# Performance work log

Hardware: AMD Instinct MI355X
Metric: run time of the kernel (lower is better)

Reference implementation:

```python
import jax, jax.numpy as jnp
import numpy as np

B, N, DIM, H, DH = 2, 2048, 1024, 16, 64
SCALE = 8.0
LN_EPS = 1e-5
L2_EPS = 1e-12


def setup_inputs() -> dict:
    key = jax.random.key(0)
    ks = jax.random.split(key, 6)
    s = 0.02  # keep projections at sane magnitude
    return {
        "x": jax.random.normal(ks[0], (B, N, DIM), dtype=jnp.float32),
        "g": jnp.ones((DIM,), dtype=jnp.float32),
        "b": jnp.zeros((DIM,), dtype=jnp.float32),
        "c_attn_w": jax.random.normal(ks[1], (DIM, 3 * DIM), dtype=jnp.float32) * s,
        "c_attn_b": jax.random.normal(ks[2], (3 * DIM,), dtype=jnp.float32) * s,
        "c_proj_w": jax.random.normal(ks[3], (DIM, DIM), dtype=jnp.float32) * s,
        "c_proj_b": jax.random.normal(ks[4], (DIM,), dtype=jnp.float32) * s,
        "to_out_w": jax.random.normal(ks[5], (DIM, DIM), dtype=jnp.float32) * s,
    }


def _l2norm(t):
    # F.normalize(t, dim=-1): t / max(||t||, eps)
    n = jnp.sqrt(jnp.sum(t * t, axis=-1, keepdims=True))
    return t / jnp.maximum(n, L2_EPS)


def reference(x, g, b, c_attn_w, c_attn_b, c_proj_w, c_proj_b, to_out_w):
    # LayerNorm
    mu = jnp.mean(x, axis=-1, keepdims=True)
    var = jnp.mean(jnp.square(x - mu), axis=-1, keepdims=True)
    y = (x - mu) * jax.lax.rsqrt(var + LN_EPS) * g + b  # [B,N,DIM]

    # GPT2 Conv1D c_attn: y @ W + b, split into q/k/v
    qkv = y @ c_attn_w + c_attn_b  # [B,N,3*DIM]
    q, k, v = jnp.split(qkv, 3, axis=-1)

    def split_heads(t):
        return t.reshape(B, N, H, DH).transpose(0, 2, 1, 3)  # [B,H,N,DH]

    q, k, v = split_heads(q), split_heads(k), split_heads(v)

    # cosine-sim attention: L2-normalize q,k, scaled dot product, causal softmax
    qn, kn = _l2norm(q), _l2norm(k)
    sim = jnp.einsum("bhid,bhjd->bhij", qn, kn) * SCALE  # [B,H,N,N]
    mask_value = -jnp.finfo(sim.dtype).max
    causal = jnp.triu(jnp.ones((N, N), dtype=bool), k=1)
    sim = jnp.where(causal, mask_value, sim)
    attn = jax.nn.softmax(sim, axis=-1)
    o = jnp.einsum("bhij,bhjd->bhid", attn, v)  # [B,H,N,DH]

    o = o.transpose(0, 2, 1, 3).reshape(B, N, DIM)
    o = o @ c_proj_w + c_proj_b          # Conv1D c_proj
    out = o @ to_out_w.T                  # Linear to_out (no bias)
    return out
```

## Files before the change

### kernel.cpp

```cpp
#include <hip/hip_runtime.h>
#include <cstdint>
#include <cstddef>

#define Bb 2
#define Nn 2048
#define DIMM 1024
#define Hh 16
#define DHh 64
#define BH (Bb*Hh)
#define MROWS (Bb*Nn)

typedef __bf16 bf16x8 __attribute__((ext_vector_type(8)));
typedef float f32x4 __attribute__((ext_vector_type(4)));
typedef short s16x4 __attribute__((ext_vector_type(4)));

__device__ __forceinline__ unsigned short f2bf(float f) {
  unsigned u = __float_as_uint(f);
  u += 0x7FFFu + ((u >> 16) & 1u);
  return (unsigned short)(u >> 16);
}
__device__ __forceinline__ unsigned short f2bf_fast(float f) {
  return (unsigned short)((__float_as_uint(f) + 0x8000u) >> 16);
}
__device__ __forceinline__ float bf2f(unsigned short s) {
  return __uint_as_float(((unsigned)s) << 16);
}

#define GLDS16(g, l) __builtin_amdgcn_global_load_lds( \
    (const __attribute__((address_space(1))) void*)(g), \
    (__attribute__((address_space(3))) void*)(l), 16, 0, 0)

__global__ __launch_bounds__(256) void prep_kernel(
    const float* __restrict__ x, const float* __restrict__ g,
    const float* __restrict__ b,
    const float* __restrict__ c_attn_w, const float* __restrict__ c_proj_w,
    const float* __restrict__ to_out_w, const float* __restrict__ c_proj_b,
    unsigned short* __restrict__ y,
    unsigned short* __restrict__ wqkv, unsigned short* __restrict__ wpbf,
    unsigned short* __restrict__ wout, float* __restrict__ bc) {
  int bid = blockIdx.x;
  int t = threadIdx.x;
  if (bid < 4096) {
    int row = bid;
    const float4* xr = (const float4*)(x + (size_t)row * DIMM);
    float4 v = xr[t];
    float s  = v.x + v.y + v.z + v.w;
    float ss = v.x*v.x + v.y*v.y + v.z*v.z + v.w*v.w;
    #pragma unroll
    for (int o = 1; o < 64; o <<= 1) { s += __shfl_xor(s, o); ss += __shfl_xor(ss, o); }
    __shared__ float red[8];
    int wv = t >> 6;
    if ((t & 63) == 0) { red[wv] = s; red[wv + 4] = ss; }
    __syncthreads();
    s  = red[0] + red[1] + red[2] + red[3];
    ss = red[4] + red[5] + red[6] + red[7];
    float mu  = s * (1.0f / DIMM);
    float var = ss * (1.0f / DIMM) - mu * mu;
    float rs  = rsqrtf(var + 1e-5f);
    float4 gv = ((const float4*)g)[t];
    float4 bv = ((const float4*)b)[t];
    ushort4 o4;
    o4.x = f2bf((v.x - mu) * rs * gv.x + bv.x);
    o4.y = f2bf((v.y - mu) * rs * gv.y + bv.y);
    o4.z = f2bf((v.z - mu) * rs * gv.z + bv.z);
    o4.w = f2bf((v.w - mu) * rs * gv.w + bv.w);
    ((ushort4*)y)[(size_t)row * 256 + t] = o4;
  } else if (bid < 7168) {
    __shared__ float tile[32][33];
    int bb = bid - 4096;
    int bx = bb % 96, by = bb / 96;
    int tx = t & 31, ty = t >> 5;
    int x2 = bx * 32 + tx;
    int y0 = by * 32;
    #pragma unroll
    for (int j = 0; j < 32; j += 8)
      tile[ty + j][tx] = c_attn_w[(size_t)(y0 + ty + j) * 3072 + x2];
    __syncthreads();
    int ox  = by * 32 + tx;
    int oy0 = bx * 32;
    #pragma unroll
    for (int j = 0; j < 32; j += 8)
      wqkv[(size_t)(oy0 + ty + j) * 1024 + ox] = f2bf(tile[tx][ty + j]);
  } else if (bid < 9216) {
    bool iswp = bid < 8192;
    int bb = bid - (iswp ? 7168 : 8192);
    const float* in = iswp ? c_proj_w : to_out_w;
    unsigned short* out = iswp ? wpbf : wout;
    int i = (bb * 256 + t) * 4;
    float4 v = *(const float4*)(in + i);
    ushort4 o;
    o.x = f2bf(v.x); o.y = f2bf(v.y); o.z = f2bf(v.z); o.w = f2bf(v.w);
    *(ushort4*)(out + i) = o;
  } else {
    int n = (bid - 9216) * 4 + (t >> 6);
    int lane = t & 63;
    const float4* w = (const float4*)(to_out_w + (size_t)n * DIMM);
    const float4* b4 = (const float4*)c_proj_b;
    float s = 0.0f;
    #pragma unroll
    for (int k = 0; k < 4; k++) {
      float4 wv = w[lane + k * 64], bv = b4[lane + k * 64];
      s += wv.x * bv.x + wv.y * bv.y + wv.z * bv.z + wv.w * bv.w;
    }
    #pragma unroll
    for (int o = 1; o < 64; o <<= 1) s += __shfl_xor(s, o);
    if (lane == 0) bc[n] = s;
  }
}

template <int EPI>
__device__ __forceinline__ void gemm_body(
    const unsigned short* __restrict__ A, const unsigned short* __restrict__ Bt,
    const float* __restrict__ bias,
    unsigned short* __restrict__ obf, float* __restrict__ of32,
    unsigned short* __restrict__ q_std, unsigned short* __restrict__ k_std,
    unsigned short* __restrict__ vt_out,
    int M, int N, int K, int bn, int bm,
    unsigned short* smem) {
  unsigned short* sA = smem;
  unsigned short* sB = smem + 128 * 64;
  int t = threadIdx.x;
  int lane = t & 63, wv = t >> 6;
  int wm = (wv >> 1) * 64, wn = (wv & 1) * 64;
  int l16 = lane & 15, quad = lane >> 4;

  const unsigned short* Ab = A + (size_t)(bm * 128) * K;
  const unsigned short* Bb2 = Bt + (size_t)(bn * 128) * K;
  int srow = t >> 3;
  int gch = (t & 7) ^ (srow & 7);

  f32x4 acc[4][4] = {};

  for (int kt = 0; kt < K; kt += 64) {
    __syncthreads();
    #pragma unroll
    for (int i = 0; i < 4; i++) {
      GLDS16(Ab  + (size_t)(srow + 32 * i) * K + kt + gch * 8, sA + (size_t)(t + 256 * i) * 8);
      GLDS16(Bb2 + (size_t)(srow + 32 * i) * K + kt + gch * 8, sB + (size_t)(t + 256 * i) * 8);
    }
    __syncthreads();
    #pragma unroll
    for (int kk = 0; kk < 2; kk++) {
      int slot = (kk * 4 + quad) ^ (l16 & 7);
      bf16x8 af[4], bfr[4];
      #pragma unroll
      for (int i = 0; i < 4; i++)
        af[i] = *(const bf16x8*)(sA + (size_t)(wm + i * 16 + l16) * 64 + slot * 8);
      #pragma unroll
      for (int j = 0; j < 4; j++)
        bfr[j] = *(const bf16x8*)(sB + (size_t)(wn + j * 16 + l16) * 64 + slot * 8);
      #pragma unroll
      for (int i = 0; i < 4; i++)
        #pragma unroll
        for (int j = 0; j < 4; j++)
          acc[i][j] = __builtin_amdgcn_mfma_f32_16x16x32_bf16(af[i], bfr[j], acc[i][j], 0, 0, 0);
    }
  }

  float bvals[4];
  #pragma unroll
  for (int j = 0; j < 4; j++)
    bvals[j] = (EPI == 3) ? 0.0f : bias[bn * 128 + wn + j * 16 + l16];

  if (EPI == 0) {
    int which = bn >> 3;
    if (which < 2) {
      #pragma unroll
      for (int i = 0; i < 4; i++) {
        #pragma unroll
        for (int r = 0; r < 4; r++) {
          int m = bm * 128 + wm + i * 16 + quad * 4 + r;
          float vals[4];
          float ss = 0.0f;
          #pragma unroll
          for (int j = 0; j < 4; j++) {
            vals[j] = acc[i][j][r] + bvals[j];
            ss += vals[j] * vals[j];
          }
          ss += __shfl_xor(ss, 1); ss += __shfl_xor(ss, 2);
          ss += __shfl_xor(ss, 4); ss += __shfl_xor(ss, 8);
          float scale = ((which == 0) ? 8.0f : 1.0f) / fmaxf(sqrtf(ss), 1e-12f);
          int bi = m >> 11, ns = m & 2047;
          unsigned short* dst = (which == 0) ? q_std : k_std;
          #pragma unroll
          for (int j = 0; j < 4; j++) {
            int n = bn * 128 + wn + j * 16 + l16;
            int nn2 = n & 1023;
            int h = nn2 >> 6, d = nn2 & 63;
            dst[((size_t)((bi * Hh + h) * Nn + ns)) * DHh + d] = f2bf(vals[j] * scale);
          }
        }
      }
    } else {
      __syncthreads();
      #pragma unroll
      for (int i = 0; i < 4; i++) {
        int mchunk = (wm + i * 16) / 4 + quad;
        #pragma unroll
        for (int j = 0; j < 4; j++) {
          int n_local = wn + j * 16 + l16;
          int sw = mchunk ^ (n_local & 31);
          ushort4 pack;
          pack.x = f2bf(acc[i][j][0] + bvals[j]);
          pack.y = f2bf(acc[i][j][1] + bvals[j]);
          pack.z = f2bf(acc[i][j][2] + bvals[j]);
          pack.w = f2bf(acc[i][j][3] + bvals[j]);
          *(ushort4*)(smem + (size_t)n_local * 128 + sw * 4) = pack;
        }
      }
      __syncthreads();
      int drow = t >> 1, mh = t & 1;
      int h = (bn - 16) * 2 + (drow >> 6);
      int d = drow & 63;
      int bi = bm >> 4;
      int ns0 = (bm * 128) & 2047;
      unsigned short* dst = vt_out + ((size_t)(bi * Hh + h) * DHh + d) * Nn + ns0 + mh * 64;
      #pragma unroll
      for (int cc = 0; cc < 16; cc++) {
        int c0 = mh * 16 + cc;
        int s0 = c0 ^ (drow & 31);
        *(ushort4*)(dst + cc * 4) = *(const ushort4*)(smem + (size_t)drow * 128 + s0 * 4);
      }
    }
  } else {
    #pragma unroll
    for (int i = 0; i < 4; i++) {
      #pragma unroll
      for (int j = 0; j < 4; j++) {
        int n = bn * 128 + wn + j * 16 + l16;
        #pragma unroll
        for (int r = 0; r < 4; r++) {
          int m = bm * 128 + wm + i * 16 + quad * 4 + r;
          float val = acc[i][j][r] + bvals[j];
          if (EPI == 2) of32[(size_t)m * N + n] = val;
          else          obf[(size_t)m * N + n] = f2bf(val);
        }
      }
    }
  }
}

__global__ __launch_bounds__(256) void gemm_qkv_wcomb(
    const unsigned short* __restrict__ y, const unsigned short* __restrict__ wqkv,
    const float* __restrict__ c_attn_b,
    unsigned short* __restrict__ q_std, unsigned short* __restrict__ k_std,
    unsigned short* __restrict__ vt_out,
    const unsigned short* __restrict__ wout, const unsigned short* __restrict__ wpbf,
    unsigned short* __restrict__ wcomb) {
  __shared__ unsigned short smem[128 * 64 * 2];
  int bn = blockIdx.x, bm = blockIdx.y;
  if (bn < 24) {
    gemm_body<0>(y, wqkv, c_attn_b, nullptr, nullptr, q_std, k_std, vt_out,
                 MROWS, 3 * DIMM, DIMM, bn, bm, smem);
  } else {
    int idx = (bn - 24) * 32 + bm;
    gemm_body<3>(wout, wpbf, nullptr, wcomb, nullptr, nullptr, nullptr, nullptr,
                 DIMM, DIMM, DIMM, idx & 7, idx >> 3, smem);
  }
}

__global__ __launch_bounds__(256) void gemm_final(
    const unsigned short* __restrict__ A, const unsigned short* __restrict__ Bt,
    const float* __restrict__ bias, float* __restrict__ of32) {
  __shared__ unsigned short smem[128 * 64 * 2];
  gemm_body<2>(A, Bt, bias, nullptr, of32, nullptr, nullptr, nullptr,
               MROWS, DIMM, DIMM, blockIdx.x, blockIdx.y, smem);
}

__global__ __launch_bounds__(512, 4) void attn_kernel(
    const unsigned short* __restrict__ qn, const unsigned short* __restrict__ kn,
    const unsigned short* __restrict__ vt, unsigned short* __restrict__ o_flat) {
  __shared__ float smemf[8704];
  int t = threadIdx.x, lane = t & 63, wv = t >> 6;
  int half = wv >> 2, strip = wv & 3;
  int l16 = lane & 15, quad = lane >> 4;
  int id = blockIdx.x;
  int qb = (id < 256) ? (15 - (id >> 5)) : ((id - 256) >> 5);
  int bh = id & 31;
  int m0 = qb * 128 + strip * 32;
  const unsigned short* qbase = qn + (size_t)bh * Nn * DHh;
  const unsigned short* kbase = kn + (size_t)bh * Nn * DHh;
  const unsigned short* vbase = vt + (size_t)bh * DHh * Nn;

  unsigned short* myK = (unsigned short*)((char*)smemf + half * 16384);
  unsigned short* myV = (unsigned short*)((char*)smemf + half * 16384 + 8192);

  bf16x8 aq[2][2];
  #pragma unroll
  for (int i2 = 0; i2 < 2; i2++)
    #pragma unroll
    for (int kk = 0; kk < 2; kk++)
      aq[i2][kk] = *(const bf16x8*)(qbase + (size_t)(m0 + i2 * 16 + l16) * DHh + kk * 32 + quad * 8);

  f32x4 accOT[4][2] = {};
  float den[2] = {};

  int tl = t & 255;
  int srow = tl >> 3;
  int gch = (tl & 7) ^ (srow & 7);
  int nh = qb + 1;
  int kt0 = half * nh;

  for (int kt = 0; kt < nh; kt++) {
    int j0 = (kt0 + kt) * 64;
    __syncthreads();
    GLDS16(kbase + (size_t)(j0 + srow)      * DHh + gch * 8, myK + (size_t)tl * 8);
    GLDS16(kbase + (size_t)(j0 + srow + 32) * DHh + gch * 8, myK + (size_t)(tl + 256) * 8);
    GLDS16(vbase + (size_t)srow        * Nn + j0 + gch * 8, myV + (size_t)tl * 8);
    GLDS16(vbase + (size_t)(srow + 32) * Nn + j0 + gch * 8, myV + (size_t)(tl + 256) * 8);
    __syncthreads();

    if (j0 > m0 + 31) continue;

    f32x4 sc[4][2] = {};
    #pragma unroll
    for (int kk = 0; kk < 2; kk++) {
      int slot = (kk * 4 + quad) ^ (l16 & 7);
      #pragma unroll
      for (int jt = 0; jt < 4; jt++) {
        bf16x8 ak = *(const bf16x8*)(myK + (size_t)(jt * 16 + l16) * 64 + slot * 8);
        #pragma unroll
        for (int i2 = 0; i2 < 2; i2++)
          sc[jt][i2] = __builtin_amdgcn_mfma_f32_16x16x32_bf16(ak, aq[i2][kk], sc[jt][i2], 0, 0, 0);
      }
    }

    bool fullTile = (j0 + 63) <= m0;
    s16x4 pf[4][2];
    #pragma unroll
    for (int jt = 0; jt < 4; jt++) {
      #pragma unroll
      for (int i2 = 0; i2 < 2; i2++) {
        int m = m0 + i2 * 16 + l16;
        #pragma unroll
        for (int r = 0; r < 4; r++) {
          int j = j0 + jt * 16 + quad * 4 + r;
          float p;
          if (fullTile) p = __expf(sc[jt][i2][r] - 8.0f);
          else          p = (j <= m) ? __expf(sc[jt][i2][r] - 8.0f) : 0.0f;
          den[i2] += p;
          pf[jt][i2][r] = (short)f2bf_fast(p);
        }
      }
    }

    #pragma unroll
    for (int jt = 0; jt < 4; jt++) {
      #pragma unroll
      for (int dt = 0; dt < 4; dt++) {
        int row = dt * 16 + l16;
        int ch = (jt * 2 + (quad >> 1)) ^ (l16 & 7);
        s16x4 av = *(const s16x4*)(myV + (size_t)row * 64 + ch * 8 + (quad & 1) * 4);
        #pragma unroll
        for (int i2 = 0; i2 < 2; i2++)
          accOT[dt][i2] = __builtin_amdgcn_mfma_f32_16x16x16bf16_1k(av, pf[jt][i2], accOT[dt][i2], 0, 0, 0);
      }
    }
  }

  #pragma unroll
  for (int i2 = 0; i2 < 2; i2++) {
    float d = den[i2];
    d += __shfl_xor(d, 16); d += __shfl_xor(d, 32);
    den[i2] = d;
  }

  __syncthreads();
  float* scr = smemf + strip * 2176;
  if (half == 1) {
    #pragma unroll
    for (int dt = 0; dt < 4; dt++)
      #pragma unroll
      for (int i2 = 0; i2 < 2; i2++)
        *(f32x4*)(scr + ((size_t)(dt * 2 + i2) * 64 + lane) * 4) = accOT[dt][i2];
    scr[2048 + lane] = den[0];
    scr[2048 + 64 + lane] = den[1];
  }
  __syncthreads();
  if (half == 0) {
    float dinv[2];
    dinv[0] = 1.0f / (den[0] + scr[2048 + lane]);
    dinv[1] = 1.0f / (den[1] + scr[2048 + 64 + lane]);
    int bi = bh >> 4, h = bh & 15;
    #pragma unroll
    for (int i2 = 0; i2 < 2; i2++) {
      #pragma unroll
      for (int dt = 0; dt < 4; dt++) {
        f32x4 o = accOT[dt][i2] + *(const f32x4*)(scr + ((size_t)(dt * 2 + i2) * 64 + lane) * 4);
        ushort4 o4;
        o4.x = f2bf(o[0] * dinv[i2]);
        o4.y = f2bf(o[1] * dinv[i2]);
        o4.z = f2bf(o[2] * dinv[i2]);
        o4.w = f2bf(o[3] * dinv[i2]);
        int ns = m0 + i2 * 16 + l16;
        int d0 = dt * 16 + quad * 4;
        *(ushort4*)(o_flat + ((size_t)(bi * Nn + ns)) * DIMM + h * DHh + d0) = o4;
      }
    }
  }
}

extern "C" void kernel_launch(void* const* d_in, const int* in_sizes, int n_in,
                              void* d_out, int out_size, void* d_ws, size_t ws_size,
                              hipStream_t stream) {
  const float* x        = (const float*)d_in[0];
  const float* g        = (const float*)d_in[1];
  const float* b        = (const float*)d_in[2];
  const float* c_attn_w = (const float*)d_in[3];
  const float* c_attn_b = (const float*)d_in[4];
  const float* c_proj_w = (const float*)d_in[5];
  const float* c_proj_b = (const float*)d_in[6];
  const float* to_out_w = (const float*)d_in[7];
  float* out = (float*)d_out;

  char* p = (char*)d_ws;
  unsigned short* y     = (unsigned short*)(p + ((size_t)0  << 20));
  unsigned short* qbuf  = (unsigned short*)(p + ((size_t)8  << 20));
  unsigned short* kbuf  = (unsigned short*)(p + ((size_t)16 << 20));
  unsigned short* vtb   = (unsigned short*)(p + ((size_t)24 << 20));
  unsigned short* wpbf  = (unsigned short*)(p + ((size_t)32 << 20));
  unsigned short* wout  = (unsigned short*)(p + ((size_t)34 << 20));
  unsigned short* wqkv  = (unsigned short*)(p + ((size_t)40 << 20));
  unsigned short* wcomb = (unsigned short*)(p + ((size_t)46 << 20));
  float*          bc    = (float*)        (p + ((size_t)48 << 20));

  prep_kernel<<<9472, 256, 0, stream>>>(x, g, b, c_attn_w, c_proj_w, to_out_w,
                                        c_proj_b, y, wqkv, wpbf, wout, bc);
  gemm_qkv_wcomb<<<dim3(26, MROWS / 128), 256, 0, stream>>>(
      y, wqkv, c_attn_b, qbuf, kbuf, vtb, wout, wpbf, wcomb);
  attn_kernel<<<512, 512, 0, stream>>>(qbuf, kbuf, vtb, y);
  gemm_final<<<dim3(DIMM / 128, MROWS / 128), 256, 0, stream>>>(y, wcomb, bc, out);
}
```

Baseline: 206.7 us.

## Double-buffer GEMM LDS tiles with async prefetch two stages ahead

Converts the shared GEMM body from a single-buffered load-sync-compute loop into a two-buffer pipeline. Global-to-LDS loads for tile k+2 are issued while tile k is consumed, and partial vmcnt waits replace the full syncs. MFMA sections are also raised in wave priority. This doubles LDS use per block to 64KB, which may lower occupancy, and depends on the hand-tuned vmcnt count matching the number of loads in flight.

```diff
diff --git a/kernel.cpp b/kernel.cpp
--- a/kernel.cpp
+++ b/kernel.cpp
@@ -117,8 +117,6 @@
     unsigned short* __restrict__ vt_out,
     int M, int N, int K, int bn, int bm,
     unsigned short* smem) {
-  unsigned short* sA = smem;
-  unsigned short* sB = smem + 128 * 64;
   int t = threadIdx.x;
   int lane = t & 63, wv = t >> 6;
   int wm = (wv >> 1) * 64, wn = (wv & 1) * 64;
@@ -130,15 +128,30 @@
   int gch = (t & 7) ^ (srow & 7);
 
   f32x4 acc[4][4] = {};
-
-  for (int kt = 0; kt < K; kt += 64) {
-    __syncthreads();
+  const int KT = K >> 6;
+
+  auto stage = [&](int kt_, int b_) {
+    unsigned short* dA = smem + b_ * 16384;
+    unsigned short* dB = dA + 8192;
+    const unsigned short* gA = Ab  + (size_t)srow * K + kt_ * 64 + gch * 8;
+    const unsigned short* gB = Bb2 + (size_t)srow * K + kt_ * 64 + gch * 8;
     #pragma unroll
     for (int i = 0; i < 4; i++) {
-      GLDS16(Ab  + (size_t)(srow + 32 * i) * K + kt + gch * 8, sA + (size_t)(t + 256 * i) * 8);
-      GLDS16(Bb2 + (size_t)(srow + 32 * i) * K + kt + gch * 8, sB + (size_t)(t + 256 * i) * 8);
-    }
-    __syncthreads();
+      GLDS16(gA + (size_t)(32 * i) * K, dA + (size_t)(t + 256 * i) * 8);
+      GLDS16(gB + (size_t)(32 * i) * K, dB + (size_t)(t + 256 * i) * 8);
+    }
+  };
+
+  stage(0, 0);
+  if (KT > 1) stage(1, 1);
+
+  for (int kt2 = 0; kt2 < KT; ++kt2) {
+    if (kt2 < KT - 1) asm volatile("s_waitcnt vmcnt(8)" ::: "memory");
+    else              asm volatile("s_waitcnt vmcnt(0)" ::: "memory");
+    __builtin_amdgcn_s_barrier();
+    __builtin_amdgcn_sched_barrier(0);
+    const unsigned short* sA = smem + (kt2 & 1) * 16384;
+    const unsigned short* sB = sA + 8192;
     #pragma unroll
     for (int kk = 0; kk < 2; kk++) {
       int slot = (kk * 4 + quad) ^ (l16 & 7);
@@ -149,12 +162,18 @@
       #pragma unroll
       for (int j = 0; j < 4; j++)
         bfr[j] = *(const bf16x8*)(sB + (size_t)(wn + j * 16 + l16) * 64 + slot * 8);
+      __builtin_amdgcn_s_setprio(1);
       #pragma unroll
       for (int i = 0; i < 4; i++)
         #pragma unroll
         for (int j = 0; j < 4; j++)
           acc[i][j] = __builtin_amdgcn_mfma_f32_16x16x32_bf16(af[i], bfr[j], acc[i][j], 0, 0, 0);
-    }
+      __builtin_amdgcn_s_setprio(0);
+    }
+    __builtin_amdgcn_sched_barrier(0);
+    __builtin_amdgcn_s_barrier();
+    __builtin_amdgcn_sched_barrier(0);
+    if (kt2 + 2 < KT) stage(kt2 + 2, kt2 & 1);
   }
 
   float bvals[4];
@@ -247,7 +266,7 @@
     unsigned short* __restrict__ vt_out,
     const unsigned short* __restrict__ wout, const unsigned short* __restrict__ wpbf,
     unsigned short* __restrict__ wcomb) {
-  __shared__ unsigned short smem[128 * 64 * 2];
+  __shared__ unsigned short smem[32768];
   int bn = blockIdx.x, bm = blockIdx.y;
   if (bn < 24) {
     gemm_body<0>(y, wqkv, c_attn_b, nullptr, nullptr, q_std, k_std, vt_out,
@@ -262,7 +281,7 @@
 __global__ __launch_bounds__(256) void gemm_final(
     const unsigned short* __restrict__ A, const unsigned short* __restrict__ Bt,
     const float* __restrict__ bias, float* __restrict__ of32) {
-  __shared__ unsigned short smem[128 * 64 * 2];
+  __shared__ unsigned short smem[32768];
   gemm_body<2>(A, Bt, bias, nullptr, of32, nullptr, nullptr, nullptr,
                MROWS, DIMM, DIMM, blockIdx.x, blockIdx.y, smem);
 }
```

New measurement: 200.1 us. -3.2%, faster.
